# Optimization experiments

Hardware: AMD Instinct MI355X
Metric: run time of the kernel (lower is better)

## Reference

```python
import jax, jax.numpy as jnp
import numpy as np

N_TOP = 5  # self.n from __init__
EPS = 1e-10


def setup_inputs() -> dict:
    key = jax.random.key(0)
    k1, k2 = jax.random.split(key)
    support_set = jax.random.normal(k1, (8, 4096, 64), dtype=jnp.float32)
    query_set = jax.random.normal(k2, (8, 4096, 64), dtype=jnp.float32)
    return {"support_set": support_set, "query_set": query_set, "bshot": 2048}


def reference(support_set, query_set, bshot):
    # support_set: [B,S,D], query_set: [B,Q,D]
    sum_support = jnp.sum(support_set * support_set, axis=2)          # [B,S]
    support_magnitude = jax.lax.rsqrt(jnp.clip(sum_support, EPS))     # clamp(eps, inf).rsqrt()
    dot = jnp.einsum('bqd,bsd->bqs', query_set, support_set)          # [B,Q,S]
    cos = dot * support_magnitude[:, None, :]                         # scale per support column
    top_vals, _ = jax.lax.top_k(cos[:, :, :bshot], N_TOP)             # [B,Q,n]
    return jnp.concatenate([top_vals, cos[:, :, bshot:]], axis=2)     # [B,Q,n+(S-bshot)]
```

## Files before the change

### kernel.cpp

```cpp
#include <hip/hip_runtime.h>
#include <hip/hip_bf16.h>

#define B_ 8
#define S_ 4096
#define Q_ 4096
#define D_ 64

typedef __attribute__((ext_vector_type(8))) short short8;
typedef __attribute__((ext_vector_type(4))) float f32x4;

__device__ __forceinline__ unsigned short f2bf(float f) {
  union { float f; unsigned u; } v; v.f = f;
  unsigned u = v.u;
  u += 0x7FFFu + ((u >> 16) & 1u);
  return (unsigned short)(u >> 16);
}

__global__ void prep_kernel(const float* __restrict__ supp,
                            const float* __restrict__ query,
                            unsigned short* __restrict__ supp_bf,
                            unsigned short* __restrict__ query_bf) {
  int r = blockIdx.x * blockDim.x + threadIdx.x;
  const int nsupp = B_ * S_;
  const int total = nsupp + B_ * Q_;
  if (r >= total) return;
  const bool is_supp = r < nsupp;
  const float* src = is_supp ? (supp + (size_t)r * D_)
                             : (query + (size_t)(r - nsupp) * D_);
  unsigned short* dst = is_supp ? (supp_bf + (size_t)r * D_)
                                : (query_bf + (size_t)(r - nsupp) * D_);
  float4 v[D_ / 4];
  float sum = 0.f;
#pragma unroll
  for (int i = 0; i < D_ / 4; ++i) {
    v[i] = ((const float4*)src)[i];
    sum += v[i].x * v[i].x + v[i].y * v[i].y + v[i].z * v[i].z + v[i].w * v[i].w;
  }
  const float sc = is_supp ? rsqrtf(fmaxf(sum, 1e-10f)) : 1.0f;
#pragma unroll
  for (int i = 0; i < D_ / 4; ++i) {
    ushort4 h;
    h.x = f2bf(v[i].x * sc); h.y = f2bf(v[i].y * sc);
    h.z = f2bf(v[i].z * sc); h.w = f2bf(v[i].w * sc);
    ((ushort4*)dst)[i] = h;
  }
}

__device__ __forceinline__ void ins5(float (&t)[5], float v) {
  float a = v, b;
  b = fminf(t[0], a); t[0] = fmaxf(t[0], a); a = b;
  b = fminf(t[1], a); t[1] = fmaxf(t[1], a); a = b;
  b = fminf(t[2], a); t[2] = fmaxf(t[2], a); a = b;
  b = fminf(t[3], a); t[3] = fmaxf(t[3], a); a = b;
  t[4] = fmaxf(t[4], a);
}

__global__ void cos_topk_kernel(const unsigned short* __restrict__ supp_bf,
                                const unsigned short* __restrict__ query_bf,
                                const int* __restrict__ pbshot,
                                float* __restrict__ out) {
  const int bs = *pbshot;
  const int OW = 5 + S_ - bs;

  const int b  = blockIdx.x >> 6;
  const int q0 = (blockIdx.x & 63) * 64;
  const int tid  = threadIdx.x;
  const int w    = tid >> 6;
  const int lane = tid & 63;
  const int l15  = lane & 15;
  const int l4   = lane >> 4;

  const int nt_top = bs >> 6;
  const int role = blockIdx.y;
  const bool is_top = (role == 0);
  int t0, t1;
  if (is_top) { t0 = 0; t1 = nt_top; }
  else {
    const int ct = (S_ >> 6) - nt_top;
    t0 = nt_top + (ct * (role - 1)) / 3;
    t1 = nt_top + (ct * role) / 3;
  }

  __shared__ unsigned short lds[2][64 * 64];

  const int qrow = q0 + w * 16 + l15;
  const unsigned short* qbase = query_bf + (size_t)(b * Q_ + qrow) * D_;
  const short8 a0 = *(const short8*)(qbase + l4 * 8);
  const short8 a1 = *(const short8*)(qbase + 32 + l4 * 8);

  float tk[4][5];
#pragma unroll
  for (int r2 = 0; r2 < 4; ++r2)
#pragma unroll
    for (int j = 0; j < 5; ++j) tk[r2][j] = -INFINITY;

  const int srow  = tid >> 2;
  const int chunk = tid & 3;
  const unsigned short* gstage0 =
      supp_bf + ((size_t)b * S_ + srow) * D_ + chunk * 16;
  const int dsw0 = srow * 64 + ((chunk * 16 + 0) ^ ((srow & 7) << 3));
  const int dsw1 = srow * 64 + ((chunk * 16 + 8) ^ ((srow & 7) << 3));

  uint4 st0 = *(const uint4*)(gstage0 + (size_t)t0 * 64 * D_);
  uint4 st1 = *(const uint4*)(gstage0 + (size_t)t0 * 64 * D_ + 8);
  *(uint4*)&lds[0][dsw0] = st0;
  *(uint4*)&lds[0][dsw1] = st1;

  const int rbase = b * Q_ + q0 + w * 16 + l4 * 4;
  float* obase = out + (size_t)rbase * OW + 5 - bs;

  for (int t = t0; t < t1; ++t) {
    const int buf = (t - t0) & 1;
    if (t + 1 < t1) {
      const unsigned short* g = gstage0 + (size_t)(t + 1) * 64 * D_;
      st0 = *(const uint4*)(g);
      st1 = *(const uint4*)(g + 8);
    }
    __syncthreads();

#pragma unroll
    for (int fc = 0; fc < 4; ++fc) {
      const int scol = fc * 16 + l15;
      const int idx0 = scol * 64 + ((l4 * 8) ^ ((scol & 7) << 3));
      const int idx1 = scol * 64 + ((32 + l4 * 8) ^ ((scol & 7) << 3));
      const short8 b0 = *(const short8*)&lds[buf][idx0];
      const short8 b1 = *(const short8*)&lds[buf][idx1];
      f32x4 acc = {0.f, 0.f, 0.f, 0.f};
      acc = __builtin_amdgcn_mfma_f32_16x16x32_bf16(a0, b0, acc, 0, 0, 0);
      acc = __builtin_amdgcn_mfma_f32_16x16x32_bf16(a1, b1, acc, 0, 0, 0);

      const int col = t * 64 + fc * 16 + l15;
      if (is_top) {
#pragma unroll
        for (int r2 = 0; r2 < 4; ++r2) ins5(tk[r2], acc[r2]);
      } else {
        float* op = obase + col;
#pragma unroll
        for (int r2 = 0; r2 < 4; ++r2) op[(size_t)r2 * OW] = acc[r2];
      }
    }

    if (t + 1 < t1) {
      *(uint4*)&lds[buf ^ 1][dsw0] = st0;
      *(uint4*)&lds[buf ^ 1][dsw1] = st1;
    }
  }

  if (is_top) {
#pragma unroll
    for (int m = 1; m <= 8; m <<= 1) {
#pragma unroll
      for (int r2 = 0; r2 < 4; ++r2) {
        float o0 = __shfl_xor(tk[r2][0], m);
        float o1 = __shfl_xor(tk[r2][1], m);
        float o2 = __shfl_xor(tk[r2][2], m);
        float o3 = __shfl_xor(tk[r2][3], m);
        float o4 = __shfl_xor(tk[r2][4], m);
        ins5(tk[r2], o0); ins5(tk[r2], o1); ins5(tk[r2], o2);
        ins5(tk[r2], o3); ins5(tk[r2], o4);
      }
    }
    if (l15 == 0) {
#pragma unroll
      for (int r2 = 0; r2 < 4; ++r2) {
        float* op = out + (size_t)(rbase + r2) * OW;
        op[0] = tk[r2][0]; op[1] = tk[r2][1]; op[2] = tk[r2][2];
        op[3] = tk[r2][3]; op[4] = tk[r2][4];
      }
    }
  }
}

extern "C" void kernel_launch(void* const* d_in, const int* in_sizes, int n_in,
                              void* d_out, int out_size, void* d_ws, size_t ws_size,
                              hipStream_t stream) {
  const float* supp  = (const float*)d_in[0];
  const float* query = (const float*)d_in[1];
  const int* pbshot  = (const int*)d_in[2];
  float* out = (float*)d_out;

  unsigned short* supp_bf  = (unsigned short*)d_ws;
  unsigned short* query_bf = supp_bf + (size_t)B_ * S_ * D_;

  const int rows = B_ * (S_ + Q_);
  prep_kernel<<<(rows + 255) / 256, 256, 0, stream>>>(supp, query, supp_bf,
                                                      query_bf);
  dim3 grid(B_ * (Q_ / 64), 4);
  cos_topk_kernel<<<grid, 256, 0, stream>>>(supp_bf, query_bf, pbshot, out);
}
```

Before: 93.45 us.

## Load support fragments directly from global memory, drop LDS staging; nontemporal output stores

Removes the double-buffered LDS staging of support tiles and the per-tile __syncthreads. Each wave now reads its MFMA B fragments straight from global memory, relying on L1/L2 to serve the reuse across the four waves. Output stores in the non-top blocks become nontemporal to reduce cache pollution from the large streamed output. The cost is redundant global/L2 traffic, since every wave reloads the same support rows, and load latency is no longer hidden by explicit prefetch.

```diff
diff --git a/kernel.cpp b/kernel.cpp
--- a/kernel.cpp
+++ b/kernel.cpp
@@ -81,8 +81,6 @@
     t1 = nt_top + (ct * role) / 3;
   }
 
-  __shared__ unsigned short lds[2][64 * 64];
-
   const int qrow = q0 + w * 16 + l15;
   const unsigned short* qbase = query_bf + (size_t)(b * Q_ + qrow) * D_;
   const short8 a0 = *(const short8*)(qbase + l4 * 8);
@@ -94,37 +92,19 @@
 #pragma unroll
     for (int j = 0; j < 5; ++j) tk[r2][j] = -INFINITY;
 
-  const int srow  = tid >> 2;
-  const int chunk = tid & 3;
-  const unsigned short* gstage0 =
-      supp_bf + ((size_t)b * S_ + srow) * D_ + chunk * 16;
-  const int dsw0 = srow * 64 + ((chunk * 16 + 0) ^ ((srow & 7) << 3));
-  const int dsw1 = srow * 64 + ((chunk * 16 + 8) ^ ((srow & 7) << 3));
-
-  uint4 st0 = *(const uint4*)(gstage0 + (size_t)t0 * 64 * D_);
-  uint4 st1 = *(const uint4*)(gstage0 + (size_t)t0 * 64 * D_ + 8);
-  *(uint4*)&lds[0][dsw0] = st0;
-  *(uint4*)&lds[0][dsw1] = st1;
+  const unsigned short* sfrag =
+      supp_bf + ((size_t)b * S_ + l15) * D_ + l4 * 8;
 
   const int rbase = b * Q_ + q0 + w * 16 + l4 * 4;
   float* obase = out + (size_t)rbase * OW + 5 - bs;
 
   for (int t = t0; t < t1; ++t) {
-    const int buf = (t - t0) & 1;
-    if (t + 1 < t1) {
-      const unsigned short* g = gstage0 + (size_t)(t + 1) * 64 * D_;
-      st0 = *(const uint4*)(g);
-      st1 = *(const uint4*)(g + 8);
-    }
-    __syncthreads();
-
+    const unsigned short* tb = sfrag + (size_t)t * 64 * D_;
 #pragma unroll
     for (int fc = 0; fc < 4; ++fc) {
-      const int scol = fc * 16 + l15;
-      const int idx0 = scol * 64 + ((l4 * 8) ^ ((scol & 7) << 3));
-      const int idx1 = scol * 64 + ((32 + l4 * 8) ^ ((scol & 7) << 3));
-      const short8 b0 = *(const short8*)&lds[buf][idx0];
-      const short8 b1 = *(const short8*)&lds[buf][idx1];
+      const unsigned short* rowp = tb + fc * 16 * D_;
+      const short8 b0 = *(const short8*)(rowp);
+      const short8 b1 = *(const short8*)(rowp + 32);
       f32x4 acc = {0.f, 0.f, 0.f, 0.f};
       acc = __builtin_amdgcn_mfma_f32_16x16x32_bf16(a0, b0, acc, 0, 0, 0);
       acc = __builtin_amdgcn_mfma_f32_16x16x32_bf16(a1, b1, acc, 0, 0, 0);
@@ -136,13 +116,9 @@
       } else {
         float* op = obase + col;
 #pragma unroll
-        for (int r2 = 0; r2 < 4; ++r2) op[(size_t)r2 * OW] = acc[r2];
+        for (int r2 = 0; r2 < 4; ++r2)
+          __builtin_nontemporal_store(acc[r2], op + (size_t)r2 * OW);
       }
-    }
-
-    if (t + 1 < t1) {
-      *(uint4*)&lds[buf ^ 1][dsw0] = st0;
-      *(uint4*)&lds[buf ^ 1][dsw1] = st1;
     }
   }
 
```

Result: slower. 356.9 us (+281.9%).
